# Kernel optimization log

Measured on AMD Instinct MI355X. Metric: run time of the kernel, lower is better.

## Reference

```python
import jax, jax.numpy as jnp
import numpy as np

T = 2048
N = 4096
DT = 0.01
V_RESET = 1.0
ALPHA = 0.01
MAX_SPIKES = 128


def setup_inputs() -> dict:
    key = jax.random.key(0)
    ks = jax.random.split(key, 8)
    ts = jnp.arange(T, dtype=jnp.float32) * DT
    input_current = jax.random.normal(ks[0], (T, N), dtype=jnp.float32)
    # _build_w: uniform(minval=0.5) fully-connected weight matrix
    w = jax.random.uniform(ks[1], (N, N), dtype=jnp.float32, minval=0.5, maxval=1.0)
    # _build_initial: uniform(maxval=0.1)
    v0 = jax.random.uniform(ks[2], (N,), dtype=jnp.float32, maxval=0.1)
    i0 = jax.random.uniform(ks[3], (N,), dtype=jnp.float32, maxval=0.1)
    mu = jax.random.uniform(ks[4], (2,), dtype=jnp.float32, minval=0.5, maxval=1.0)
    # uniforms for initial s and for post-spike s resampling (s = log(u) - alpha)
    s0_u = jax.random.uniform(ks[5], (N,), dtype=jnp.float32)
    resample_u = jax.random.uniform(ks[6], (T, N), dtype=jnp.float32)
    return {"ts": ts, "input_current": input_current, "w": w, "v0": v0,
            "i0": i0, "mu": mu, "s0_u": s0_u, "resample_u": resample_u,
            "max_spikes": MAX_SPIKES}


def reference(ts, input_current, w, v0, i0, mu, s0_u, resample_u, max_spikes):
    """Event-driven spiking net: Euler integration of the drift vf with
    spike events when s crosses 0, followed by the masked per-neuron jump
    transition (_inner_trans_fn) using the firing neuron's weight row.
    Returns trajectory ys [T, N, 3] (v, i, s per neuron)."""
    dt = ts[1] - ts[0]
    eps = jnp.float32(1e-12)
    # s0 = log(uniform) - alpha  (always negative; drifts up at rate intensity(v))
    s0 = jnp.log(s0_u + eps) - ALPHA
    y0 = jnp.stack([v0, i0, s0], axis=-1)  # [N, 3]
    mu1, mu2 = mu[0], mu[1]

    def step(carry, xs):
        y, nsp = carry
        inp_t, ru_t = xs
        v, i, s = y[:, 0], y[:, 1], y[:, 2]
        # drift_vf (Euler step)
        v_n = v + dt * (mu1 * (i - v) + mu1 * inp_t)
        i_n = i + dt * (-mu2 * i)
        s_n = s + dt * jax.nn.sigmoid(v)  # intensity_fn(v)
        # event detection: cond_fn = s; event when s reaches 0
        ev = s_n >= 0.0  # [N] event mask
        fire = jnp.any(ev) & (nsp < max_spikes)
        idx = jnp.argmax(ev)  # event_idx = argmax over event mask
        w_row = w[idx]  # weights from firing neuron to all neurons
        # _inner_trans_fn: spiking neurons reset v and resample s;
        # non-spiking neurons receive current injection w[idx][j]
        v_t = jnp.where(ev, v_n - V_RESET, v_n)
        i_t = jnp.where(ev, i_n, i_n + w_row)
        s_t = jnp.where(ev, jnp.log(ru_t + eps) - ALPHA, s_n)
        y_fire = jnp.stack([v_t, i_t, s_t], axis=-1)
        y_free = jnp.stack([v_n, i_n, s_n], axis=-1)
        y_out = jnp.where(fire, y_fire, y_free)
        nsp = nsp + fire.astype(jnp.int32)
        return (y_out, nsp), y_out

    (_, _), ys = jax.lax.scan(step, (y0, jnp.int32(0)),
                              (input_current, resample_u))
    return ys
```

## Files before the change

kernel.cpp:

```cpp
#include <hip/hip_runtime.h>
#include <stddef.h>

#define TT 2048
#define NN 4096
#define LSEG 64
#define NSEG (TT / LSEG)
#define ABLK 16
#define ATPB 1024
#define NPT 4
#define TPB 256
#define NOFIRE 0xFFFFFFFEu

__global__ __launch_bounds__(ATPB) void phaseA(
    const float* __restrict__ ts, const float* __restrict__ inp,
    const float* __restrict__ w, const float* __restrict__ v0,
    const float* __restrict__ i0, const float* __restrict__ mu,
    const float* __restrict__ s0u, const float* __restrict__ ru,
    const int* __restrict__ mx, float* __restrict__ ys,
    unsigned int* __restrict__ hdr)
{
#pragma clang fp contract(off)
  const int tid = threadIdx.x;
  const int bid = blockIdx.x;
  const float dt = ts[1] - ts[0];
  const float mu1 = mu[0], mu2 = mu[1];
  const int maxs = mx[0];

  const int kw = bid >> 2;
  const bool wr = ((tid >> 8) == (bid & 3));
  const int nw = bid * 256 + (tid & 255);

  float v[NPT], ci[NPT], s[NPT], wv[NPT], inpv[NPT], ruv[NPT];
  bool aw[NPT];
#pragma unroll
  for (int k = 0; k < NPT; ++k) {
    int n = tid + k * ATPB;
    v[k] = v0[n];
    ci[k] = i0[n];
    s[k] = logf(s0u[n] + 1e-12f) - 0.01f;
    wv[k] = 0.0f; aw[k] = false;
    inpv[k] = inp[n];
    ruv[k]  = ru[n];
  }
  int nsp = 0, t_stop = TT;

  __shared__ unsigned int sh_w[2][ATPB / 64];

  for (int t = 0; t < TT; ++t) {
    float inpn[NPT], run[NPT];
    if (t + 1 < TT) {
#pragma unroll
      for (int k = 0; k < NPT; ++k) {
        size_t o = (size_t)(t + 1) * NN + tid + k * ATPB;
        inpn[k] = inp[o]; run[k] = ru[o];
      }
    } else {
#pragma unroll
      for (int k = 0; k < NPT; ++k) { inpn[k] = 0.0f; run[k] = 0.0f; }
    }

    float sn[NPT]; bool ev[NPT];
    unsigned int m = NOFIRE;
#pragma unroll
    for (int k = 0; k < NPT; ++k) {
      float sig = 1.0f / (1.0f + expf(-v[k]));
      sn[k] = s[k] + dt * sig;
      ev[k] = sn[k] >= 0.0f;
      unsigned int cand = ev[k] ? (unsigned int)(tid + k * ATPB) : NOFIRE;
      m = m < cand ? m : cand;
    }

    bool coupled = (nsp < maxs);
    unsigned int gm = NOFIRE;
    if (coupled) {
#pragma unroll
      for (int off = 32; off > 0; off >>= 1) {
        unsigned int o = (unsigned int)__shfl_down((int)m, off, 64);
        m = m < o ? m : o;
      }
      if ((tid & 63) == 0) sh_w[t & 1][tid >> 6] = m;
      __syncthreads();
      unsigned int bm = sh_w[t & 1][0];
#pragma unroll
      for (int j = 1; j < ATPB / 64; ++j) {
        unsigned int x = sh_w[t & 1][j];
        bm = bm < x ? bm : x;
      }
      gm = bm;
    }

    float fi[NPT];
#pragma unroll
    for (int k = 0; k < NPT; ++k) fi[k] = aw[k] ? (ci[k] + wv[k]) : ci[k];

    if (t > 0 && wr) {
      size_t o = ((size_t)(t - 1) * NN + nw) * 3;
      ys[o] = v[kw]; ys[o + 1] = fi[kw]; ys[o + 2] = s[kw];
    }

    float vn[NPT], in_[NPT];
#pragma unroll
    for (int k = 0; k < NPT; ++k) {
      vn[k] = v[k] + dt * (mu1 * (fi[k] - v[k]) + mu1 * inpv[k]);
      in_[k] = fi[k] + dt * (-mu2 * fi[k]);
    }

    bool fire = coupled && (gm < (unsigned int)NN);
#pragma unroll
    for (int k = 0; k < NPT; ++k) aw[k] = false;
    if (fire) {
      ++nsp;
#pragma unroll
      for (int k = 0; k < NPT; ++k)
        wv[k] = w[(size_t)gm * NN + tid + k * ATPB];
#pragma unroll
      for (int k = 0; k < NPT; ++k) {
        if (ev[k]) { v[k] = vn[k] - 1.0f; s[k] = logf(ruv[k] + 1e-12f) - 0.01f; }
        else       { v[k] = vn[k]; s[k] = sn[k]; aw[k] = true; }
      }
    } else {
#pragma unroll
      for (int k = 0; k < NPT; ++k) { v[k] = vn[k]; s[k] = sn[k]; }
    }
#pragma unroll
    for (int k = 0; k < NPT; ++k) { ci[k] = in_[k]; inpv[k] = inpn[k]; ruv[k] = run[k]; }

    if (nsp >= maxs && ((t + 1) & (LSEG - 1)) == 0) { t_stop = t + 1; break; }
  }

  if (wr) {
    float f = aw[kw] ? (ci[kw] + wv[kw]) : ci[kw];
    size_t o = ((size_t)(t_stop - 1) * NN + nw) * 3;
    ys[o] = v[kw]; ys[o + 1] = f; ys[o + 2] = s[kw];
  }
  if (bid == 0 && tid == 0) hdr[0] = (unsigned int)t_stop;
}

__global__ __launch_bounds__(TPB) void p1_segc(
    const float* __restrict__ ts, const float* __restrict__ inp,
    const float* __restrict__ mu, const float* __restrict__ ys,
    const unsigned int* __restrict__ hdr, float* __restrict__ buf1)
{
  unsigned int Kp = hdr[0];
  unsigned int g0 = Kp / LSEG;
  unsigned int g = blockIdx.x >> 4;
  if (g < g0) return;
  int n = (blockIdx.x & 15) * TPB + threadIdx.x;
  float dt = ts[1] - ts[0];
  float mu1 = mu[0], mu2 = mu[1];
  float a = 1.0f - dt * mu1, b = dt * mu1, r = 1.0f - dt * mu2;
  float ibase = ys[((size_t)(Kp - 1) * NN + n) * 3 + 1];
  float ij = ibase * powf(r, (float)((int)(g * LSEG) - (int)Kp));
  float c = 0.0f;
  size_t base = (size_t)(g * LSEG) * NN + n;
  for (int j = 0; j < LSEG; ++j) {
    float x = inp[base + (size_t)j * NN];
    c = a * c + b * (ij + x);
    ij *= r;
  }
  buf1[(size_t)g * NN + n] = c;
}

__global__ __launch_bounds__(TPB) void p2_scanv(
    const float* __restrict__ ts, const float* __restrict__ mu,
    const float* __restrict__ ys, const unsigned int* __restrict__ hdr,
    float* __restrict__ buf1)
{
  unsigned int Kp = hdr[0];
  unsigned int g0 = Kp / LSEG;
  if (g0 >= NSEG) return;
  int n = blockIdx.x * TPB + threadIdx.x;
  float dt = ts[1] - ts[0];
  float mu1 = mu[0];
  float a = 1.0f - dt * mu1;
  float aL = a;
  for (int k = 0; k < 6; ++k) aL *= aL;
  float v = ys[((size_t)(Kp - 1) * NN + n) * 3 + 0];
  for (unsigned int g = g0; g < NSEG; ++g) {
    float cg = buf1[(size_t)g * NN + n];
    buf1[(size_t)g * NN + n] = v;
    v = aL * v + cg;
  }
}

__global__ __launch_bounds__(TPB) void p3a_sigma(
    const float* __restrict__ ts, const float* __restrict__ inp,
    const float* __restrict__ mu, const unsigned int* __restrict__ hdr,
    const float* __restrict__ buf1, const float* __restrict__ ys,
    float* __restrict__ buf2)
{
  unsigned int Kp = hdr[0];
  unsigned int g0 = Kp / LSEG;
  unsigned int g = blockIdx.x >> 4;
  if (g < g0) return;
  int n = (blockIdx.x & 15) * TPB + threadIdx.x;
  float dt = ts[1] - ts[0];
  float mu1 = mu[0], mu2 = mu[1];
  float r = 1.0f - dt * mu2;
  float v = buf1[(size_t)g * NN + n];
  float ibase = ys[((size_t)(Kp - 1) * NN + n) * 3 + 1];
  float i = ibase * powf(r, (float)((int)(g * LSEG) - (int)Kp));
  float sl = 0.0f;
  size_t base = (size_t)(g * LSEG) * NN + n;
  for (int j = 0; j < LSEG; ++j) {
    float x = inp[base + (size_t)j * NN];
    float sig = 1.0f / (1.0f + expf(-v));
    sl = sl + dt * sig;
    float vn = v + dt * (mu1 * (i - v) + mu1 * x);
    float in_ = i + dt * (-mu2 * i);
    v = vn; i = in_;
  }
  buf2[(size_t)g * NN + n] = sl;
}

__global__ __launch_bounds__(TPB) void p4_scans(
    const float* __restrict__ ys, const unsigned int* __restrict__ hdr,
    float* __restrict__ buf2)
{
  unsigned int Kp = hdr[0];
  unsigned int g0 = Kp / LSEG;
  if (g0 >= NSEG) return;
  int n = blockIdx.x * TPB + threadIdx.x;
  float s = ys[((size_t)(Kp - 1) * NN + n) * 3 + 2];
  for (unsigned int g = g0; g < NSEG; ++g) {
    float t = buf2[(size_t)g * NN + n];
    buf2[(size_t)g * NN + n] = s;
    s += t;
  }
}

__global__ __launch_bounds__(TPB) void p3b_write(
    const float* __restrict__ ts, const float* __restrict__ inp,
    const float* __restrict__ mu, const unsigned int* __restrict__ hdr,
    const float* __restrict__ buf1, const float* __restrict__ buf2,
    const float* __restrict__ ysr, float* __restrict__ ys)
{
  unsigned int Kp = hdr[0];
  unsigned int g0 = Kp / LSEG;
  unsigned int g = blockIdx.x >> 4;
  if (g < g0) return;
  int n = (blockIdx.x & 15) * TPB + threadIdx.x;
  float dt = ts[1] - ts[0];
  float mu1 = mu[0], mu2 = mu[1];
  float r = 1.0f - dt * mu2;
  float v = buf1[(size_t)g * NN + n];
  float s = buf2[(size_t)g * NN + n];
  float ibase = ysr[((size_t)(Kp - 1) * NN + n) * 3 + 1];
  float i = ibase * powf(r, (float)((int)(g * LSEG) - (int)Kp));
  for (int j = 0; j < LSEG; ++j) {
    size_t t = (size_t)g * LSEG + j;
    float x = inp[t * NN + n];
    float sig = 1.0f / (1.0f + expf(-v));
    s = s + dt * sig;
    float vn = v + dt * (mu1 * (i - v) + mu1 * x);
    float in_ = i + dt * (-mu2 * i);
    size_t o = (t * NN + n) * 3;
    ys[o] = vn; ys[o + 1] = in_; ys[o + 2] = s;
    v = vn; i = in_;
  }
}

extern "C" void kernel_launch(void* const* d_in, const int* in_sizes, int n_in,
                              void* d_out, int out_size, void* d_ws, size_t ws_size,
                              hipStream_t stream)
{
  (void)in_sizes; (void)n_in; (void)out_size; (void)ws_size;
  const float* ts  = (const float*)d_in[0];
  const float* inp = (const float*)d_in[1];
  const float* w   = (const float*)d_in[2];
  const float* v0  = (const float*)d_in[3];
  const float* i0  = (const float*)d_in[4];
  const float* mu  = (const float*)d_in[5];
  const float* s0u = (const float*)d_in[6];
  const float* ru  = (const float*)d_in[7];
  const int*   mx  = (const int*)d_in[8];
  float* ys = (float*)d_out;

  char* wsb = (char*)d_ws;
  unsigned int* hdr = (unsigned int*)wsb;
  float* buf1 = (float*)(wsb + 1024);
  float* buf2 = buf1 + (size_t)NSEG * NN;

  phaseA<<<ABLK, ATPB, 0, stream>>>(ts, inp, w, v0, i0, mu, s0u, ru, mx, ys, hdr);
  p1_segc<<<NSEG * 16, TPB, 0, stream>>>(ts, inp, mu, ys, hdr, buf1);
  p2_scanv<<<NN / TPB, TPB, 0, stream>>>(ts, mu, ys, hdr, buf1);
  p3a_sigma<<<NSEG * 16, TPB, 0, stream>>>(ts, inp, mu, hdr, buf1, ys, buf2);
  p4_scans<<<NN / TPB, TPB, 0, stream>>>(ys, hdr, buf2);
  p3b_write<<<NSEG * 16, TPB, 0, stream>>>(ts, inp, mu, hdr, buf1, buf2, ys, ys);
}
```

Baseline: 595.8 us.

## Run serial phase in one block with float4 I/O and precomputed resample logs

The serial spiking phase drops from 16 redundant blocks to a single 1024-thread block. Each thread now owns 4 contiguous neurons and uses float4 loads and stores, including the interleaved ys writes. The per-step block reduction becomes one shared atomicMin into a triple-buffered slot, which removes the second serial pass over wave minima. A pre-kernel computes log(resample)-alpha for the first 256 rows into the tail of the output buffer, taking logf off the serial critical path. The parallel segment kernels also switch to 4 neurons per thread with vectorized loads and stores. Risks: staging the logs in the output tail relies on those rows being overwritten later, and the 16-block redundancy that may have helped latency is gone.

```diff
diff --git a/kernel.cpp b/kernel.cpp
--- a/kernel.cpp
+++ b/kernel.cpp
@@ -5,58 +5,78 @@
 #define NN 4096
 #define LSEG 64
 #define NSEG (TT / LSEG)
-#define ABLK 16
 #define ATPB 1024
 #define NPT 4
 #define TPB 256
+#define TPBB 128
 #define NOFIRE 0xFFFFFFFEu
+#define LRROWS 256
+
+__global__ __launch_bounds__(TPB) void plog_k(const float* __restrict__ ru,
+                                              float* __restrict__ lr) {
+  int idx = blockIdx.x * TPB + threadIdx.x;
+  const float4 x = ((const float4*)ru)[idx];
+  float4 y;
+  y.x = logf(x.x + 1e-12f) - 0.01f;
+  y.y = logf(x.y + 1e-12f) - 0.01f;
+  y.z = logf(x.z + 1e-12f) - 0.01f;
+  y.w = logf(x.w + 1e-12f) - 0.01f;
+  ((float4*)lr)[idx] = y;
+}
 
 __global__ __launch_bounds__(ATPB) void phaseA(
     const float* __restrict__ ts, const float* __restrict__ inp,
     const float* __restrict__ w, const float* __restrict__ v0,
     const float* __restrict__ i0, const float* __restrict__ mu,
     const float* __restrict__ s0u, const float* __restrict__ ru,
-    const int* __restrict__ mx, float* __restrict__ ys,
-    unsigned int* __restrict__ hdr)
+    const float* __restrict__ lr, const int* __restrict__ mx,
+    float* __restrict__ ys, unsigned int* __restrict__ hdr)
 {
 #pragma clang fp contract(off)
   const int tid = threadIdx.x;
-  const int bid = blockIdx.x;
+  const int nb = tid * NPT;
   const float dt = ts[1] - ts[0];
   const float mu1 = mu[0], mu2 = mu[1];
   const int maxs = mx[0];
 
-  const int kw = bid >> 2;
-  const bool wr = ((tid >> 8) == (bid & 3));
-  const int nw = bid * 256 + (tid & 255);
-
-  float v[NPT], ci[NPT], s[NPT], wv[NPT], inpv[NPT], ruv[NPT];
+  float v[NPT], ci[NPT], s[NPT], wv[NPT], inpc[NPT], lvc[NPT];
   bool aw[NPT];
-#pragma unroll
-  for (int k = 0; k < NPT; ++k) {
-    int n = tid + k * ATPB;
-    v[k] = v0[n];
-    ci[k] = i0[n];
-    s[k] = logf(s0u[n] + 1e-12f) - 0.01f;
-    wv[k] = 0.0f; aw[k] = false;
-    inpv[k] = inp[n];
-    ruv[k]  = ru[n];
-  }
+  {
+    const float4 a = *(const float4*)(v0 + nb);
+    const float4 b = *(const float4*)(i0 + nb);
+    const float4 c = *(const float4*)(s0u + nb);
+    const float4 d = *(const float4*)(inp + nb);
+    const float4 e = *(const float4*)(lr + nb);
+    v[0]=a.x; v[1]=a.y; v[2]=a.z; v[3]=a.w;
+    ci[0]=b.x; ci[1]=b.y; ci[2]=b.z; ci[3]=b.w;
+    s[0]=logf(c.x+1e-12f)-0.01f; s[1]=logf(c.y+1e-12f)-0.01f;
+    s[2]=logf(c.z+1e-12f)-0.01f; s[3]=logf(c.w+1e-12f)-0.01f;
+    inpc[0]=d.x; inpc[1]=d.y; inpc[2]=d.z; inpc[3]=d.w;
+    lvc[0]=e.x; lvc[1]=e.y; lvc[2]=e.z; lvc[3]=e.w;
+  }
+  bool logged = true;
+#pragma unroll
+  for (int k = 0; k < NPT; ++k) { wv[k] = 0.0f; aw[k] = false; }
+
+  __shared__ unsigned int slot[3];
+  if (tid < 3) slot[tid] = NOFIRE;
+  __syncthreads();
+
   int nsp = 0, t_stop = TT;
 
-  __shared__ unsigned int sh_w[2][ATPB / 64];
-
   for (int t = 0; t < TT; ++t) {
-    float inpn[NPT], run[NPT];
+    float inpn[NPT], lvn[NPT];
+    bool logged_n = false;
     if (t + 1 < TT) {
-#pragma unroll
-      for (int k = 0; k < NPT; ++k) {
-        size_t o = (size_t)(t + 1) * NN + tid + k * ATPB;
-        inpn[k] = inp[o]; run[k] = ru[o];
-      }
+      const float4 x = *(const float4*)(inp + (size_t)(t + 1) * NN + nb);
+      logged_n = (t + 1) < LRROWS;
+      const float* lp = logged_n ? lr : ru;
+      const float4 y = *(const float4*)(lp + (size_t)(t + 1) * NN + nb);
+      inpn[0]=x.x; inpn[1]=x.y; inpn[2]=x.z; inpn[3]=x.w;
+      lvn[0]=y.x; lvn[1]=y.y; lvn[2]=y.z; lvn[3]=y.w;
     } else {
 #pragma unroll
-      for (int k = 0; k < NPT; ++k) { inpn[k] = 0.0f; run[k] = 0.0f; }
+      for (int k = 0; k < NPT; ++k) { inpn[k] = 0.0f; lvn[k] = 0.0f; }
     }
 
     float sn[NPT]; bool ev[NPT];
@@ -66,99 +86,106 @@
       float sig = 1.0f / (1.0f + expf(-v[k]));
       sn[k] = s[k] + dt * sig;
       ev[k] = sn[k] >= 0.0f;
-      unsigned int cand = ev[k] ? (unsigned int)(tid + k * ATPB) : NOFIRE;
-      m = m < cand ? m : cand;
-    }
-
-    bool coupled = (nsp < maxs);
-    unsigned int gm = NOFIRE;
+      unsigned int c = ev[k] ? (unsigned int)(nb + k) : NOFIRE;
+      m = m < c ? m : c;
+    }
+    const bool coupled = (nsp < maxs);
     if (coupled) {
 #pragma unroll
       for (int off = 32; off > 0; off >>= 1) {
         unsigned int o = (unsigned int)__shfl_down((int)m, off, 64);
         m = m < o ? m : o;
       }
-      if ((tid & 63) == 0) sh_w[t & 1][tid >> 6] = m;
+      if ((tid & 63) == 0) atomicMin(&slot[t % 3], m);
+    }
+
+    float fi[NPT];
+#pragma unroll
+    for (int k = 0; k < NPT; ++k) fi[k] = aw[k] ? (ci[k] + wv[k]) : ci[k];
+    if (t > 0) {
+      float4* o = (float4*)(ys + ((size_t)(t - 1) * NN + nb) * 3);
+      o[0] = make_float4(v[0], fi[0], s[0], v[1]);
+      o[1] = make_float4(fi[1], s[1], v[2], fi[2]);
+      o[2] = make_float4(s[2], v[3], fi[3], s[3]);
+    }
+    float vn[NPT], in_[NPT];
+#pragma unroll
+    for (int k = 0; k < NPT; ++k) {
+      vn[k]  = v[k] + dt * (mu1 * (fi[k] - v[k]) + mu1 * inpc[k]);
+      in_[k] = fi[k] + dt * (-mu2 * fi[k]);
+    }
+
+    unsigned int gm = NOFIRE;
+    if (coupled) {
       __syncthreads();
-      unsigned int bm = sh_w[t & 1][0];
-#pragma unroll
-      for (int j = 1; j < ATPB / 64; ++j) {
-        unsigned int x = sh_w[t & 1][j];
-        bm = bm < x ? bm : x;
-      }
-      gm = bm;
-    }
-
-    float fi[NPT];
-#pragma unroll
-    for (int k = 0; k < NPT; ++k) fi[k] = aw[k] ? (ci[k] + wv[k]) : ci[k];
-
-    if (t > 0 && wr) {
-      size_t o = ((size_t)(t - 1) * NN + nw) * 3;
-      ys[o] = v[kw]; ys[o + 1] = fi[kw]; ys[o + 2] = s[kw];
-    }
-
-    float vn[NPT], in_[NPT];
-#pragma unroll
-    for (int k = 0; k < NPT; ++k) {
-      vn[k] = v[k] + dt * (mu1 * (fi[k] - v[k]) + mu1 * inpv[k]);
-      in_[k] = fi[k] + dt * (-mu2 * fi[k]);
-    }
-
-    bool fire = coupled && (gm < (unsigned int)NN);
+      gm = slot[t % 3];
+      if (tid == 0) slot[(t + 2) % 3] = NOFIRE;
+    }
+
+    const bool fire = coupled && (gm < (unsigned int)NN);
 #pragma unroll
     for (int k = 0; k < NPT; ++k) aw[k] = false;
     if (fire) {
       ++nsp;
-#pragma unroll
-      for (int k = 0; k < NPT; ++k)
-        wv[k] = w[(size_t)gm * NN + tid + k * ATPB];
+      const float4 wr4 = *(const float4*)(w + (size_t)gm * NN + nb);
+      wv[0]=wr4.x; wv[1]=wr4.y; wv[2]=wr4.z; wv[3]=wr4.w;
 #pragma unroll
       for (int k = 0; k < NPT; ++k) {
-        if (ev[k]) { v[k] = vn[k] - 1.0f; s[k] = logf(ruv[k] + 1e-12f) - 0.01f; }
-        else       { v[k] = vn[k]; s[k] = sn[k]; aw[k] = true; }
+        if (ev[k]) {
+          v[k] = vn[k] - 1.0f;
+          s[k] = logged ? lvc[k] : (logf(lvc[k] + 1e-12f) - 0.01f);
+        } else { v[k] = vn[k]; s[k] = sn[k]; aw[k] = true; }
       }
     } else {
 #pragma unroll
       for (int k = 0; k < NPT; ++k) { v[k] = vn[k]; s[k] = sn[k]; }
     }
 #pragma unroll
-    for (int k = 0; k < NPT; ++k) { ci[k] = in_[k]; inpv[k] = inpn[k]; ruv[k] = run[k]; }
+    for (int k = 0; k < NPT; ++k) { ci[k] = in_[k]; inpc[k] = inpn[k]; lvc[k] = lvn[k]; }
+    logged = logged_n;
 
     if (nsp >= maxs && ((t + 1) & (LSEG - 1)) == 0) { t_stop = t + 1; break; }
   }
 
-  if (wr) {
-    float f = aw[kw] ? (ci[kw] + wv[kw]) : ci[kw];
-    size_t o = ((size_t)(t_stop - 1) * NN + nw) * 3;
-    ys[o] = v[kw]; ys[o + 1] = f; ys[o + 2] = s[kw];
-  }
-  if (bid == 0 && tid == 0) hdr[0] = (unsigned int)t_stop;
-}
-
-__global__ __launch_bounds__(TPB) void p1_segc(
+  {
+    float fi[NPT];
+#pragma unroll
+    for (int k = 0; k < NPT; ++k) fi[k] = aw[k] ? (ci[k] + wv[k]) : ci[k];
+    float4* o = (float4*)(ys + ((size_t)(t_stop - 1) * NN + nb) * 3);
+    o[0] = make_float4(v[0], fi[0], s[0], v[1]);
+    o[1] = make_float4(fi[1], s[1], v[2], fi[2]);
+    o[2] = make_float4(s[2], v[3], fi[3], s[3]);
+  }
+  if (tid == 0) hdr[0] = (unsigned int)t_stop;
+}
+
+__global__ __launch_bounds__(TPBB) void p1_segc(
     const float* __restrict__ ts, const float* __restrict__ inp,
     const float* __restrict__ mu, const float* __restrict__ ys,
     const unsigned int* __restrict__ hdr, float* __restrict__ buf1)
 {
-  unsigned int Kp = hdr[0];
-  unsigned int g0 = Kp / LSEG;
-  unsigned int g = blockIdx.x >> 4;
+  const unsigned int Kp = hdr[0];
+  const unsigned int g0 = Kp / LSEG;
+  const unsigned int g = blockIdx.x >> 3;
   if (g < g0) return;
-  int n = (blockIdx.x & 15) * TPB + threadIdx.x;
-  float dt = ts[1] - ts[0];
-  float mu1 = mu[0], mu2 = mu[1];
-  float a = 1.0f - dt * mu1, b = dt * mu1, r = 1.0f - dt * mu2;
-  float ibase = ys[((size_t)(Kp - 1) * NN + n) * 3 + 1];
-  float ij = ibase * powf(r, (float)((int)(g * LSEG) - (int)Kp));
-  float c = 0.0f;
-  size_t base = (size_t)(g * LSEG) * NN + n;
+  const int nb = ((int)(blockIdx.x & 7) * TPBB + threadIdx.x) * 4;
+  const float dt = ts[1] - ts[0];
+  const float mu1 = mu[0], mu2 = mu[1];
+  const float a = 1.0f - dt * mu1, b = dt * mu1, r = 1.0f - dt * mu2;
+  const float4* yb = (const float4*)(ys + ((size_t)(Kp - 1) * NN + nb) * 3);
+  const float4 y0 = yb[0], y1 = yb[1], y2 = yb[2];
+  const float pw = powf(r, (float)((int)(g * LSEG) - (int)Kp));
+  float ij[4] = { y0.y * pw, y1.x * pw, y1.w * pw, y2.z * pw };
+  float c[4] = {0.f, 0.f, 0.f, 0.f};
+  const float* base = inp + (size_t)g * LSEG * NN + nb;
   for (int j = 0; j < LSEG; ++j) {
-    float x = inp[base + (size_t)j * NN];
-    c = a * c + b * (ij + x);
-    ij *= r;
-  }
-  buf1[(size_t)g * NN + n] = c;
+    const float4 x = *(const float4*)(base + (size_t)j * NN);
+    c[0] = a * c[0] + b * (ij[0] + x.x); ij[0] *= r;
+    c[1] = a * c[1] + b * (ij[1] + x.y); ij[1] *= r;
+    c[2] = a * c[2] + b * (ij[2] + x.z); ij[2] *= r;
+    c[3] = a * c[3] + b * (ij[3] + x.w); ij[3] *= r;
+  }
+  *(float4*)(buf1 + (size_t)g * NN + nb) = make_float4(c[0], c[1], c[2], c[3]);
 }
 
 __global__ __launch_bounds__(TPB) void p2_scanv(
@@ -166,16 +193,15 @@
     const float* __restrict__ ys, const unsigned int* __restrict__ hdr,
     float* __restrict__ buf1)
 {
-  unsigned int Kp = hdr[0];
-  unsigned int g0 = Kp / LSEG;
+  const unsigned int Kp = hdr[0];
+  const unsigned int g0 = Kp / LSEG;
   if (g0 >= NSEG) return;
-  int n = blockIdx.x * TPB + threadIdx.x;
-  float dt = ts[1] - ts[0];
-  float mu1 = mu[0];
-  float a = 1.0f - dt * mu1;
+  const int n = blockIdx.x * TPB + threadIdx.x;
+  const float dt = ts[1] - ts[0];
+  const float a = 1.0f - dt * mu[0];
   float aL = a;
   for (int k = 0; k < 6; ++k) aL *= aL;
-  float v = ys[((size_t)(Kp - 1) * NN + n) * 3 + 0];
+  float v = ys[((size_t)(Kp - 1) * NN + n) * 3];
   for (unsigned int g = g0; g < NSEG; ++g) {
     float cg = buf1[(size_t)g * NN + n];
     buf1[(size_t)g * NN + n] = v;
@@ -183,44 +209,51 @@
   }
 }
 
-__global__ __launch_bounds__(TPB) void p3a_sigma(
+__global__ __launch_bounds__(TPBB) void p3a_sigma(
     const float* __restrict__ ts, const float* __restrict__ inp,
     const float* __restrict__ mu, const unsigned int* __restrict__ hdr,
     const float* __restrict__ buf1, const float* __restrict__ ys,
     float* __restrict__ buf2)
 {
-  unsigned int Kp = hdr[0];
-  unsigned int g0 = Kp / LSEG;
-  unsigned int g = blockIdx.x >> 4;
+  const unsigned int Kp = hdr[0];
+  const unsigned int g0 = Kp / LSEG;
+  const unsigned int g = blockIdx.x >> 3;
   if (g < g0) return;
-  int n = (blockIdx.x & 15) * TPB + threadIdx.x;
-  float dt = ts[1] - ts[0];
-  float mu1 = mu[0], mu2 = mu[1];
-  float r = 1.0f - dt * mu2;
-  float v = buf1[(size_t)g * NN + n];
-  float ibase = ys[((size_t)(Kp - 1) * NN + n) * 3 + 1];
-  float i = ibase * powf(r, (float)((int)(g * LSEG) - (int)Kp));
-  float sl = 0.0f;
-  size_t base = (size_t)(g * LSEG) * NN + n;
+  const int nb = ((int)(blockIdx.x & 7) * TPBB + threadIdx.x) * 4;
+  const float dt = ts[1] - ts[0];
+  const float mu1 = mu[0], mu2 = mu[1];
+  const float r = 1.0f - dt * mu2;
+  const float4 vb = *(const float4*)(buf1 + (size_t)g * NN + nb);
+  float v[4] = { vb.x, vb.y, vb.z, vb.w };
+  const float4* yb = (const float4*)(ys + ((size_t)(Kp - 1) * NN + nb) * 3);
+  const float4 y0 = yb[0], y1 = yb[1], y2 = yb[2];
+  const float pw = powf(r, (float)((int)(g * LSEG) - (int)Kp));
+  float i[4] = { y0.y * pw, y1.x * pw, y1.w * pw, y2.z * pw };
+  float sl[4] = {0.f, 0.f, 0.f, 0.f};
+  const float* base = inp + (size_t)g * LSEG * NN + nb;
   for (int j = 0; j < LSEG; ++j) {
-    float x = inp[base + (size_t)j * NN];
-    float sig = 1.0f / (1.0f + expf(-v));
-    sl = sl + dt * sig;
-    float vn = v + dt * (mu1 * (i - v) + mu1 * x);
-    float in_ = i + dt * (-mu2 * i);
-    v = vn; i = in_;
-  }
-  buf2[(size_t)g * NN + n] = sl;
+    const float4 x = *(const float4*)(base + (size_t)j * NN);
+    float xx[4] = { x.x, x.y, x.z, x.w };
+#pragma unroll
+    for (int k = 0; k < 4; ++k) {
+      float sig = 1.0f / (1.0f + expf(-v[k]));
+      sl[k] = sl[k] + dt * sig;
+      float vn = v[k] + dt * (mu1 * (i[k] - v[k]) + mu1 * xx[k]);
+      float in_ = i[k] + dt * (-mu2 * i[k]);
+      v[k] = vn; i[k] = in_;
+    }
+  }
+  *(float4*)(buf2 + (size_t)g * NN + nb) = make_float4(sl[0], sl[1], sl[2], sl[3]);
 }
 
 __global__ __launch_bounds__(TPB) void p4_scans(
     const float* __restrict__ ys, const unsigned int* __restrict__ hdr,
     float* __restrict__ buf2)
 {
-  unsigned int Kp = hdr[0];
-  unsigned int g0 = Kp / LSEG;
+  const unsigned int Kp = hdr[0];
+  const unsigned int g0 = Kp / LSEG;
   if (g0 >= NSEG) return;
-  int n = blockIdx.x * TPB + threadIdx.x;
+  const int n = blockIdx.x * TPB + threadIdx.x;
   float s = ys[((size_t)(Kp - 1) * NN + n) * 3 + 2];
   for (unsigned int g = g0; g < NSEG; ++g) {
     float t = buf2[(size_t)g * NN + n];
@@ -229,34 +262,46 @@
   }
 }
 
-__global__ __launch_bounds__(TPB) void p3b_write(
+__global__ __launch_bounds__(TPBB) void p3b_write(
     const float* __restrict__ ts, const float* __restrict__ inp,
     const float* __restrict__ mu, const unsigned int* __restrict__ hdr,
     const float* __restrict__ buf1, const float* __restrict__ buf2,
-    const float* __restrict__ ysr, float* __restrict__ ys)
-{
-  unsigned int Kp = hdr[0];
-  unsigned int g0 = Kp / LSEG;
-  unsigned int g = blockIdx.x >> 4;
+    float* __restrict__ ys)
+{
+  const unsigned int Kp = hdr[0];
+  const unsigned int g0 = Kp / LSEG;
+  const unsigned int g = blockIdx.x >> 3;
   if (g < g0) return;
-  int n = (blockIdx.x & 15) * TPB + threadIdx.x;
-  float dt = ts[1] - ts[0];
-  float mu1 = mu[0], mu2 = mu[1];
-  float r = 1.0f - dt * mu2;
-  float v = buf1[(size_t)g * NN + n];
-  float s = buf2[(size_t)g * NN + n];
-  float ibase = ysr[((size_t)(Kp - 1) * NN + n) * 3 + 1];
-  float i = ibase * powf(r, (float)((int)(g * LSEG) - (int)Kp));
+  const int nb = ((int)(blockIdx.x & 7) * TPBB + threadIdx.x) * 4;
+  const float dt = ts[1] - ts[0];
+  const float mu1 = mu[0], mu2 = mu[1];
+  const float r = 1.0f - dt * mu2;
+  const float4 vb = *(const float4*)(buf1 + (size_t)g * NN + nb);
+  const float4 sb = *(const float4*)(buf2 + (size_t)g * NN + nb);
+  float v[4] = { vb.x, vb.y, vb.z, vb.w };
+  float s[4] = { sb.x, sb.y, sb.z, sb.w };
+  const float4* yb = (const float4*)(ys + ((size_t)(Kp - 1) * NN + nb) * 3);
+  const float4 y0 = yb[0], y1 = yb[1], y2 = yb[2];
+  const float pw = powf(r, (float)((int)(g * LSEG) - (int)Kp));
+  float i[4] = { y0.y * pw, y1.x * pw, y1.w * pw, y2.z * pw };
+  const float* base = inp + (size_t)g * LSEG * NN + nb;
   for (int j = 0; j < LSEG; ++j) {
-    size_t t = (size_t)g * LSEG + j;
-    float x = inp[t * NN + n];
-    float sig = 1.0f / (1.0f + expf(-v));
-    s = s + dt * sig;
-    float vn = v + dt * (mu1 * (i - v) + mu1 * x);
-    float in_ = i + dt * (-mu2 * i);
-    size_t o = (t * NN + n) * 3;
-    ys[o] = vn; ys[o + 1] = in_; ys[o + 2] = s;
-    v = vn; i = in_;
+    const float4 x = *(const float4*)(base + (size_t)j * NN);
+    float xx[4] = { x.x, x.y, x.z, x.w };
+    float vn[4], in_[4];
+#pragma unroll
+    for (int k = 0; k < 4; ++k) {
+      float sig = 1.0f / (1.0f + expf(-v[k]));
+      s[k] = s[k] + dt * sig;
+      vn[k] = v[k] + dt * (mu1 * (i[k] - v[k]) + mu1 * xx[k]);
+      in_[k] = i[k] + dt * (-mu2 * i[k]);
+    }
+    float4* o = (float4*)(ys + (((size_t)g * LSEG + j) * NN + nb) * 3);
+    o[0] = make_float4(vn[0], in_[0], s[0], vn[1]);
+    o[1] = make_float4(in_[1], s[1], vn[2], in_[2]);
+    o[2] = make_float4(s[2], vn[3], in_[3], s[3]);
+#pragma unroll
+    for (int k = 0; k < 4; ++k) { v[k] = vn[k]; i[k] = in_[k]; }
   }
 }
 
@@ -281,10 +326,13 @@
   float* buf1 = (float*)(wsb + 1024);
   float* buf2 = buf1 + (size_t)NSEG * NN;
 
-  phaseA<<<ABLK, ATPB, 0, stream>>>(ts, inp, w, v0, i0, mu, s0u, ru, mx, ys, hdr);
-  p1_segc<<<NSEG * 16, TPB, 0, stream>>>(ts, inp, mu, ys, hdr, buf1);
+  float* lr = ys + (size_t)TT * NN * 3 - (size_t)LRROWS * NN;
+
+  plog_k<<<LRROWS * NN / 4 / TPB, TPB, 0, stream>>>(ru, lr);
+  phaseA<<<1, ATPB, 0, stream>>>(ts, inp, w, v0, i0, mu, s0u, ru, lr, mx, ys, hdr);
+  p1_segc<<<NSEG * 8, TPBB, 0, stream>>>(ts, inp, mu, ys, hdr, buf1);
   p2_scanv<<<NN / TPB, TPB, 0, stream>>>(ts, mu, ys, hdr, buf1);
-  p3a_sigma<<<NSEG * 16, TPB, 0, stream>>>(ts, inp, mu, hdr, buf1, ys, buf2);
+  p3a_sigma<<<NSEG * 8, TPBB, 0, stream>>>(ts, inp, mu, hdr, buf1, ys, buf2);
   p4_scans<<<NN / TPB, TPB, 0, stream>>>(ys, hdr, buf2);
-  p3b_write<<<NSEG * 16, TPB, 0, stream>>>(ts, inp, mu, hdr, buf1, buf2, ys, ys);
-}
+  p3b_write<<<NSEG * 8, TPBB, 0, stream>>>(ts, inp, mu, hdr, buf1, buf2, ys);
+}
```

Result: slower. 736.0 us (+23.5%).
